# Kernel optimization log

Hardware: AMD Instinct MI355X
Metric: run time of the kernel (lower is better)

Reference implementation:

```python
import jax, jax.numpy as jnp
import numpy as np

B, S, D = 4, 2048, 1024


def setup_inputs() -> dict:
    key = jax.random.key(0)
    ks = jax.random.split(key, 4)
    scale = 1.0 / np.sqrt(D)
    x = jax.random.normal(ks[0], (B, S, D), dtype=jnp.float32)
    Wk = jax.random.normal(ks[1], (D, D), dtype=jnp.float32) * scale
    Wq = jax.random.normal(ks[2], (D, D), dtype=jnp.float32) * scale
    Wv = jax.random.normal(ks[3], (D, D), dtype=jnp.float32) * scale
    bk = jnp.zeros((D,), dtype=jnp.float32)
    bq = jnp.zeros((D,), dtype=jnp.float32)
    bv = jnp.zeros((D,), dtype=jnp.float32)
    return {"x": x, "Wk": Wk, "bk": bk, "Wq": Wq, "bq": bq,
            "Wv": Wv, "bv": bv, "dims": 2}


def correlated_weight(k, q, v, dims):
    # correlation between every query position and every key position,
    # scaled by sqrt(d) for numerical stability (standard correlation attn)
    d = q.shape[-1]
    scores = jnp.einsum("bqd,bkd->bqk", q, k) / jnp.sqrt(jnp.asarray(d, q.dtype))
    w = jax.nn.softmax(scores, axis=dims)          # [B, S, S]
    return jnp.einsum("bqk,bkd->bqd", w, v)        # [B, S, D]


def reference(x, Wk, bk, Wq, bq, Wv, bv, dims):
    # injected key/query/value funcs instantiated as Linear layers
    k = jnp.einsum("bsd,de->bse", x, Wk) + bk
    q = jnp.einsum("bsd,de->bse", x, Wq) + bq
    v = jnp.einsum("bsd,de->bse", x, Wv) + bv
    return correlated_weight(k, q, v, dims)
```

## Files before the change

### kernel.cpp

```cpp
#include <hip/hip_runtime.h>
#include <hip/hip_bf16.h>
#include <stdint.h>


typedef unsigned short u16;
typedef __bf16 bf16x8 __attribute__((ext_vector_type(8)));
typedef float  f32x16 __attribute__((ext_vector_type(16)));
typedef u16    u16x4  __attribute__((ext_vector_type(4)));
typedef u16    u16x8  __attribute__((ext_vector_type(8)));

__device__ __forceinline__ u16 f2bf(float f) {
  union { float f; uint32_t u; } v; v.f = f;
  uint32_t r = v.u + 0x7fffu + ((v.u >> 16) & 1u);
  return (u16)(r >> 16);
}

#define GLD_LDS16(gp, lp) __builtin_amdgcn_global_load_lds(                   \
    (const __attribute__((address_space(1))) void*)(gp),                      \
    (__attribute__((address_space(3))) void*)(lp), 16, 0, 0)


__global__ __launch_bounds__(256) void prep(const float* __restrict__ x,
                                            const float* __restrict__ Wq,
                                            const float* __restrict__ Wk,
                                            const float* __restrict__ Wv,
                                            const float* __restrict__ bq,
                                            const float* __restrict__ bk,
                                            const float* __restrict__ bv,
                                            u16* __restrict__ xb,
                                            u16* __restrict__ wt,
                                            float* __restrict__ bc,
                                            float* __restrict__ l) {
  __shared__ float t[32][33];
  const int bid = blockIdx.x;
  const int tid = threadIdx.x;
  if (bid < 8192) {
    int i = (bid * 256 + tid) * 4;
    float4 v = *(const float4*)(x + i);
    u16x4 o; o.x = f2bf(v.x); o.y = f2bf(v.y); o.z = f2bf(v.z); o.w = f2bf(v.w);
    *(u16x4*)(xb + i) = o;
  } else if (bid < 11264) {
    int b2 = bid - 8192;
    int zz = b2 >> 10, rem = b2 & 1023;
    const float* W = zz == 0 ? Wq : (zz == 1 ? Wk : Wv);
    u16* dst = wt + (size_t)zz * 1024 * 1024;
    int e0 = (rem & 31) * 32, d0 = (rem >> 5) * 32;
    int tx = tid & 31, ty = tid >> 5;
    #pragma unroll
    for (int i = 0; i < 4; ++i)
      t[ty + i * 8][tx] = W[(size_t)(d0 + ty + i * 8) * 1024 + e0 + tx];
    __syncthreads();
    #pragma unroll
    for (int i = 0; i < 4; ++i)
      dst[(size_t)(e0 + ty + i * 8) * 1024 + d0 + tx] = f2bf(t[tx][ty + i * 8]);
  } else if (bid < 11276) {
    int i = (bid - 11264) * 256 + tid;
    if (i < 3072)
      bc[i] = (i < 1024) ? bq[i] : (i < 2048 ? bk[i - 1024] : bv[i - 2048]);
  } else {
    int i = (bid - 11276) * 256 + tid;
    l[i] = 0.0f;
  }
}

__global__ __launch_bounds__(256) void trans_v(const u16* __restrict__ qkv,
                                               u16* __restrict__ vT) {
  __shared__ u16 t[64][72];
  int b = blockIdx.z;
  int s0 = blockIdx.x * 64, e0 = blockIdx.y * 64;
  const u16* src = qkv + (size_t)b * 2048 * 3072 + 2048;
  u16* dst = vT + (size_t)b * 1024 * 2048;
  int tx = threadIdx.x & 7, ty = threadIdx.x >> 3;
  #pragma unroll
  for (int rr = 0; rr < 64; rr += 32)
    *(u16x8*)&t[ty + rr][tx * 8] =
        *(const u16x8*)(src + (size_t)(s0 + ty + rr) * 3072 + e0 + tx * 8);
  __syncthreads();
  #pragma unroll
  for (int rr = 0; rr < 64; rr += 32) {
    int er = ty + rr;
    u16x8 o;
    #pragma unroll
    for (int j = 0; j < 8; ++j) o[j] = t[tx * 8 + j][er];
    *(u16x8*)(dst + (size_t)(e0 + er) * 2048 + s0 + tx * 8) = o;
  }
}


template <int BN, bool OUT_BF16, bool BIAS, bool EXPSUM, bool DIV>
__global__ __launch_bounds__(256)
void gemm_bt(const u16* __restrict__ A, int lda, long long sA,
             const u16* __restrict__ B, int ldb, long long sB,
             void* __restrict__ C, int ldc, long long sC,
             const float* __restrict__ bias, float* __restrict__ lptr,
             int K, float scale) {
  constexpr int NJ = BN / 64;
  __shared__ u16 As[128 * 64];
  __shared__ u16 Bs[BN * 64];
  const int lane = threadIdx.x & 63;
  const int wv = threadIdx.x >> 6;

  const u16* Ab = A + (size_t)blockIdx.z * sA + (size_t)blockIdx.y * 128 * lda;
  const u16* Bb = B + (size_t)blockIdx.z * sB + (size_t)blockIdx.x * BN * ldb;

  const int srow = lane >> 3;
  const int scol = ((lane & 7) ^ (lane >> 3)) * 8;
  const int r32 = lane & 31;
  const int half = lane >> 5;
  const int rx = lane & 7;
  const int wm = (wv >> 1) * 64;
  const int wn = (wv & 1) * (BN / 2);

  f32x16 acc[2][NJ];
  #pragma unroll
  for (int i = 0; i < 2; ++i)
    #pragma unroll
    for (int j = 0; j < NJ; ++j) acc[i][j] = (f32x16)0.0f;

  for (int k0 = 0; k0 < K; k0 += 64) {
    #pragma unroll
    for (int i = 0; i < 4; ++i) {
      int r = wv * 32 + i * 8;
      GLD_LDS16(Ab + (size_t)(r + srow) * lda + k0 + scol, As + r * 64);
    }
    #pragma unroll
    for (int i = 0; i < BN / 32; ++i) {
      int r = wv * (BN / 4) + i * 8;
      GLD_LDS16(Bb + (size_t)(r + srow) * ldb + k0 + scol, Bs + r * 64);
    }
    __syncthreads();

    bf16x8 af[2][4], bfr[NJ][4];
    #pragma unroll
    for (int t = 0; t < 4; ++t) {
      int pc = ((t * 2 + half) ^ rx) * 8;
      #pragma unroll
      for (int i = 0; i < 2; ++i)
        af[i][t] = *(const bf16x8*)(As + (wm + i * 32 + r32) * 64 + pc);
      #pragma unroll
      for (int j = 0; j < NJ; ++j)
        bfr[j][t] = *(const bf16x8*)(Bs + (wn + j * 32 + r32) * 64 + pc);
    }
    #pragma unroll
    for (int i = 0; i < 2; ++i)
      #pragma unroll
      for (int j = 0; j < NJ; ++j)
        #pragma unroll
        for (int t = 0; t < 4; ++t)
          acc[i][j] = __builtin_amdgcn_mfma_f32_32x32x16_bf16(
              af[i][t], bfr[j][t], acc[i][j], 0, 0, 0);
    __syncthreads();
  }

  const int ccol0 = blockIdx.x * BN + wn + r32;
  const int crow0 = blockIdx.y * 128 + wm + 4 * half;
  u16* Cb = (u16*)C + (size_t)blockIdx.z * sC;
  float* Cf = (float*)C + (size_t)blockIdx.z * sC;
  float* lz = EXPSUM ? (lptr + (size_t)blockIdx.z * 2048) : nullptr;
  const float* lin = DIV ? (bias + (size_t)blockIdx.z * 2048) : nullptr;

  #pragma unroll
  for (int i = 0; i < 2; ++i) {
    #pragma unroll
    for (int e = 0; e < 16; ++e) {
      int m = crow0 + i * 32 + (e & 3) + 8 * (e >> 2);
      float rinv;
      if (DIV) rinv = 1.0f / lin[m];
      float rp = 0.f;
      #pragma unroll
      for (int j = 0; j < NJ; ++j) {
        int n = ccol0 + j * 32;
        float v = acc[i][j][e] * scale;
        if (BIAS) v += bias[n];
        if (EXPSUM) { v = exp2f(v); rp += v; }
        if (DIV) v *= rinv;
        if (OUT_BF16) Cb[(size_t)m * ldc + n] = f2bf(v);
        else          Cf[(size_t)m * ldc + n] = v;
      }
      if (EXPSUM) {
        #pragma unroll
        for (int off = 16; off > 0; off >>= 1) rp += __shfl_xor(rp, off);
        if (r32 == 0) atomicAdd(&lz[m], rp);
      }
    }
  }
}


extern "C" void kernel_launch(void* const* d_in, const int* in_sizes, int n_in,
                              void* d_out, int out_size, void* d_ws, size_t ws_size,
                              hipStream_t stream) {
  const float* x  = (const float*)d_in[0];
  const float* Wk = (const float*)d_in[1];
  const float* bk = (const float*)d_in[2];
  const float* Wq = (const float*)d_in[3];
  const float* bq = (const float*)d_in[4];
  const float* Wv = (const float*)d_in[5];
  const float* bv = (const float*)d_in[6];
  float* out = (float*)d_out;

  char* ws = (char*)d_ws;
  u16*   xb  = (u16*)(ws + 0);
  u16*   wt  = (u16*)(ws + 16777216);
  float* bc  = (float*)(ws + 23068672);
  u16*   qkv = (u16*)(ws + 23080960);
  u16*   vT  = (u16*)(ws + 73412608);
  u16*   P   = (u16*)(ws + 90189824);
  float* l   = (float*)(ws + 123744256);
  (void)in_sizes; (void)n_in; (void)out_size; (void)ws_size;

  prep<<<11308, 256, 0, stream>>>(x, Wq, Wk, Wv, bq, bk, bv, xb, wt, bc, l);

  gemm_bt<128, true, true, false, false><<<dim3(24, 64, 1), 256, 0, stream>>>(
      xb, 1024, 0LL, wt, 1024, 0LL, (void*)qkv, 3072, 0LL, bc, nullptr,
      1024, 1.0f);

  trans_v<<<dim3(32, 16, 4), 256, 0, stream>>>(qkv, vT);

  gemm_bt<128, true, false, true, false><<<dim3(16, 16, 4), 256, 0, stream>>>(
      qkv, 3072, 2048LL * 3072, qkv + 1024, 3072, 2048LL * 3072,
      (void*)P, 2048, 2048LL * 2048, nullptr, l,
      1024, 0.03125f * 1.44269504f);

  gemm_bt<64, false, false, false, true><<<dim3(16, 16, 4), 256, 0, stream>>>(
      P, 2048, 2048LL * 2048, vT, 2048, 1024LL * 2048,
      out, 1024, 2048LL * 1024, l, nullptr,
      2048, 1.0f);
}
```

Baseline: 283.1 us.

## Use 128x128 tiles with 8 waves for PV GEMM and reduce row-sum atomics

The final P·V GEMM moves from 128x64 tiles with 4 waves to a dedicated 512-thread kernel using 128x128 tiles. This halves the block count and doubles reuse of each loaded P tile. The score GEMM now combines per-row exp sums of its two column waves in shared memory, so it issues one atomic per row per block instead of two. The risks are lower occupancy, since each PV block is larger and there are fewer of them (512 blocks), plus an extra barrier in the score epilogue.

```diff
diff --git a/kernel.cpp b/kernel.cpp
--- a/kernel.cpp
+++ b/kernel.cpp
@@ -87,21 +87,21 @@
 }
 
 
-template <int BN, bool OUT_BF16, bool BIAS, bool EXPSUM, bool DIV>
+template <bool OUT_BF16, bool BIAS, bool EXPSUM>
 __global__ __launch_bounds__(256)
 void gemm_bt(const u16* __restrict__ A, int lda, long long sA,
              const u16* __restrict__ B, int ldb, long long sB,
              void* __restrict__ C, int ldc, long long sC,
              const float* __restrict__ bias, float* __restrict__ lptr,
              int K, float scale) {
-  constexpr int NJ = BN / 64;
   __shared__ u16 As[128 * 64];
-  __shared__ u16 Bs[BN * 64];
+  __shared__ u16 Bs[128 * 64];
+  __shared__ float rsum[EXPSUM ? 128 : 1][2];
   const int lane = threadIdx.x & 63;
   const int wv = threadIdx.x >> 6;
 
   const u16* Ab = A + (size_t)blockIdx.z * sA + (size_t)blockIdx.y * 128 * lda;
-  const u16* Bb = B + (size_t)blockIdx.z * sB + (size_t)blockIdx.x * BN * ldb;
+  const u16* Bb = B + (size_t)blockIdx.z * sB + (size_t)blockIdx.x * 128 * ldb;
 
   const int srow = lane >> 3;
   const int scol = ((lane & 7) ^ (lane >> 3)) * 8;
@@ -109,42 +109,37 @@
   const int half = lane >> 5;
   const int rx = lane & 7;
   const int wm = (wv >> 1) * 64;
-  const int wn = (wv & 1) * (BN / 2);
-
-  f32x16 acc[2][NJ];
+  const int wn = (wv & 1) * 64;
+
+  f32x16 acc[2][2];
   #pragma unroll
   for (int i = 0; i < 2; ++i)
     #pragma unroll
-    for (int j = 0; j < NJ; ++j) acc[i][j] = (f32x16)0.0f;
+    for (int j = 0; j < 2; ++j) acc[i][j] = (f32x16)0.0f;
 
   for (int k0 = 0; k0 < K; k0 += 64) {
     #pragma unroll
     for (int i = 0; i < 4; ++i) {
       int r = wv * 32 + i * 8;
       GLD_LDS16(Ab + (size_t)(r + srow) * lda + k0 + scol, As + r * 64);
-    }
-    #pragma unroll
-    for (int i = 0; i < BN / 32; ++i) {
-      int r = wv * (BN / 4) + i * 8;
       GLD_LDS16(Bb + (size_t)(r + srow) * ldb + k0 + scol, Bs + r * 64);
     }
     __syncthreads();
 
-    bf16x8 af[2][4], bfr[NJ][4];
+    bf16x8 af[2][4], bfr[2][4];
     #pragma unroll
     for (int t = 0; t < 4; ++t) {
       int pc = ((t * 2 + half) ^ rx) * 8;
       #pragma unroll
-      for (int i = 0; i < 2; ++i)
-        af[i][t] = *(const bf16x8*)(As + (wm + i * 32 + r32) * 64 + pc);
-      #pragma unroll
-      for (int j = 0; j < NJ; ++j)
-        bfr[j][t] = *(const bf16x8*)(Bs + (wn + j * 32 + r32) * 64 + pc);
+      for (int i = 0; i < 2; ++i) {
+        af[i][t]  = *(const bf16x8*)(As + (wm + i * 32 + r32) * 64 + pc);
+        bfr[i][t] = *(const bf16x8*)(Bs + (wn + i * 32 + r32) * 64 + pc);
+      }
     }
     #pragma unroll
     for (int i = 0; i < 2; ++i)
       #pragma unroll
-      for (int j = 0; j < NJ; ++j)
+      for (int j = 0; j < 2; ++j)
         #pragma unroll
         for (int t = 0; t < 4; ++t)
           acc[i][j] = __builtin_amdgcn_mfma_f32_32x32x16_bf16(
@@ -152,38 +147,105 @@
     __syncthreads();
   }
 
-  const int ccol0 = blockIdx.x * BN + wn + r32;
+  const int ccol0 = blockIdx.x * 128 + wn + r32;
   const int crow0 = blockIdx.y * 128 + wm + 4 * half;
   u16* Cb = (u16*)C + (size_t)blockIdx.z * sC;
   float* Cf = (float*)C + (size_t)blockIdx.z * sC;
-  float* lz = EXPSUM ? (lptr + (size_t)blockIdx.z * 2048) : nullptr;
-  const float* lin = DIV ? (bias + (size_t)blockIdx.z * 2048) : nullptr;
 
   #pragma unroll
   for (int i = 0; i < 2; ++i) {
     #pragma unroll
     for (int e = 0; e < 16; ++e) {
-      int m = crow0 + i * 32 + (e & 3) + 8 * (e >> 2);
-      float rinv;
-      if (DIV) rinv = 1.0f / lin[m];
+      int lm = wm + i * 32 + (e & 3) + 8 * (e >> 2) + 4 * half;
+      int m = blockIdx.y * 128 + lm;
       float rp = 0.f;
       #pragma unroll
-      for (int j = 0; j < NJ; ++j) {
+      for (int j = 0; j < 2; ++j) {
         int n = ccol0 + j * 32;
         float v = acc[i][j][e] * scale;
         if (BIAS) v += bias[n];
         if (EXPSUM) { v = exp2f(v); rp += v; }
-        if (DIV) v *= rinv;
         if (OUT_BF16) Cb[(size_t)m * ldc + n] = f2bf(v);
         else          Cf[(size_t)m * ldc + n] = v;
       }
       if (EXPSUM) {
         #pragma unroll
         for (int off = 16; off > 0; off >>= 1) rp += __shfl_xor(rp, off);
-        if (r32 == 0) atomicAdd(&lz[m], rp);
+        if (r32 == 0) rsum[lm][wv & 1] = rp;
       }
     }
   }
+  if (EXPSUM) {
+    __syncthreads();
+    if (threadIdx.x < 128) {
+      float s = rsum[threadIdx.x][0] + rsum[threadIdx.x][1];
+      atomicAdd(lptr + (size_t)blockIdx.z * 2048 + blockIdx.y * 128 + threadIdx.x, s);
+    }
+  }
+  (void)crow0;
+}
+
+__global__ __launch_bounds__(512)
+void gemm_bt8(const u16* __restrict__ A, int lda, long long sA,
+              const u16* __restrict__ B, int ldb, long long sB,
+              float* __restrict__ C, int ldc, long long sC,
+              const float* __restrict__ l, int K, float scale) {
+  __shared__ u16 As[128 * 64];
+  __shared__ u16 Bs[128 * 64];
+  const int lane = threadIdx.x & 63;
+  const int wv = threadIdx.x >> 6;
+
+  const u16* Ab = A + (size_t)blockIdx.z * sA + (size_t)blockIdx.y * 128 * lda;
+  const u16* Bb = B + (size_t)blockIdx.z * sB + (size_t)blockIdx.x * 128 * ldb;
+
+  const int srow = lane >> 3;
+  const int scol = ((lane & 7) ^ (lane >> 3)) * 8;
+  const int r32 = lane & 31;
+  const int half = lane >> 5;
+  const int rx = lane & 7;
+  const int wm = (wv >> 2) * 64;
+  const int wn = (wv & 3) * 32;
+
+  f32x16 acc[2];
+  acc[0] = (f32x16)0.0f; acc[1] = (f32x16)0.0f;
+
+  for (int k0 = 0; k0 < K; k0 += 64) {
+    #pragma unroll
+    for (int i = 0; i < 2; ++i) {
+      int r = wv * 16 + i * 8;
+      GLD_LDS16(Ab + (size_t)(r + srow) * lda + k0 + scol, As + r * 64);
+      GLD_LDS16(Bb + (size_t)(r + srow) * ldb + k0 + scol, Bs + r * 64);
+    }
+    __syncthreads();
+
+    bf16x8 af[2][4], bfr[4];
+    #pragma unroll
+    for (int t = 0; t < 4; ++t) {
+      int pc = ((t * 2 + half) ^ rx) * 8;
+      af[0][t] = *(const bf16x8*)(As + (wm + r32) * 64 + pc);
+      af[1][t] = *(const bf16x8*)(As + (wm + 32 + r32) * 64 + pc);
+      bfr[t]   = *(const bf16x8*)(Bs + (wn + r32) * 64 + pc);
+    }
+    #pragma unroll
+    for (int i = 0; i < 2; ++i)
+      #pragma unroll
+      for (int t = 0; t < 4; ++t)
+        acc[i] = __builtin_amdgcn_mfma_f32_32x32x16_bf16(
+            af[i][t], bfr[t], acc[i], 0, 0, 0);
+    __syncthreads();
+  }
+
+  const int ccol = blockIdx.x * 128 + wn + r32;
+  const int crow0 = blockIdx.y * 128 + wm + 4 * half;
+  float* Cf = C + (size_t)blockIdx.z * sC;
+  const float* lz = l + (size_t)blockIdx.z * 2048;
+  #pragma unroll
+  for (int i = 0; i < 2; ++i)
+    #pragma unroll
+    for (int e = 0; e < 16; ++e) {
+      int m = crow0 + i * 32 + (e & 3) + 8 * (e >> 2);
+      Cf[(size_t)m * ldc + ccol] = acc[i][e] * scale / lz[m];
+    }
 }
 
 
@@ -211,19 +273,18 @@
 
   prep<<<11308, 256, 0, stream>>>(x, Wq, Wk, Wv, bq, bk, bv, xb, wt, bc, l);
 
-  gemm_bt<128, true, true, false, false><<<dim3(24, 64, 1), 256, 0, stream>>>(
+  gemm_bt<true, true, false><<<dim3(24, 64, 1), 256, 0, stream>>>(
       xb, 1024, 0LL, wt, 1024, 0LL, (void*)qkv, 3072, 0LL, bc, nullptr,
       1024, 1.0f);
 
   trans_v<<<dim3(32, 16, 4), 256, 0, stream>>>(qkv, vT);
 
-  gemm_bt<128, true, false, true, false><<<dim3(16, 16, 4), 256, 0, stream>>>(
+  gemm_bt<true, false, true><<<dim3(16, 16, 4), 256, 0, stream>>>(
       qkv, 3072, 2048LL * 3072, qkv + 1024, 3072, 2048LL * 3072,
       (void*)P, 2048, 2048LL * 2048, nullptr, l,
       1024, 0.03125f * 1.44269504f);
 
-  gemm_bt<64, false, false, false, true><<<dim3(16, 16, 4), 256, 0, stream>>>(
+  gemm_bt8<<<dim3(8, 16, 4), 512, 0, stream>>>(
       P, 2048, 2048LL * 2048, vT, 2048, 1024LL * 2048,
-      out, 1024, 2048LL * 1024, l, nullptr,
-      2048, 1.0f);
-}
+      out, 1024, 2048LL * 1024, l, 2048, 1.0f);
+}
```

New measurement: 277.4 us. 1.02x faster.
